# Optimization experiments

Measured on AMD Instinct MI355X. Metric: run time of the kernel, lower is better.

Reference implementation:

```python
import jax, jax.numpy as jnp
import numpy as np

RADIUS = 0.1
NSAMPLE = 32


def setup_inputs() -> dict:
    key = jax.random.key(0)
    k1, k2, k3 = jax.random.split(key, 3)
    B, N, P, C = 2, 16384, 4096, 64
    xyz = jax.random.uniform(k1, (B, N, 3), dtype=jnp.float32)
    new_xyz = jax.random.uniform(k2, (B, P, 3), dtype=jnp.float32)
    features = jax.random.normal(k3, (B, C, N), dtype=jnp.float32)
    return {"xyz": xyz, "new_xyz": new_xyz, "features": features}


def _ball_query(xyz, new_xyz, radius, nsample):
    """Return (B, npoint, nsample) int32 indices of the first `nsample` points
    (in original order) within `radius` of each query center. Slots beyond the
    number of valid neighbors are padded with the first valid index (0 if none),
    matching the standard PointNet++ CUDA ball_query semantics."""
    N = xyz.shape[1]
    # squared distances [B, P, N]
    d2 = jnp.sum((new_xyz[:, :, None, :] - xyz[:, None, :, :]) ** 2, axis=-1)
    in_ball = d2 < (radius * radius)
    # score = point index if in ball, else N (sentinel); smallest nsample scores
    # are the first nsample in-ball indices in original order.
    score = jnp.where(in_ball, jnp.arange(N, dtype=jnp.int32), jnp.int32(N))
    neg_topk, _ = jax.lax.top_k(-score, nsample)  # largest of -score == smallest score
    idx = -neg_topk  # [B, P, nsample], ascending
    first = idx[..., :1]
    idx = jnp.where(idx >= N, first, idx)  # pad invalid slots with first valid
    idx = jnp.where(idx >= N, 0, idx)      # no neighbor at all -> 0
    return idx


def _group(features, idx):
    """features (B, C, N), idx (B, P, S) -> (B, C, P, S)"""
    return jax.vmap(lambda f, i: f[:, i])(features, idx)


def reference(xyz, new_xyz, features):
    idx = _ball_query(xyz, new_xyz, RADIUS, NSAMPLE)          # (B, P, S)
    xyz_t = jnp.transpose(xyz, (0, 2, 1))                      # (B, 3, N)
    grouped_xyz = _group(xyz_t, idx)                           # (B, 3, P, S)
    grouped_xyz = grouped_xyz - jnp.transpose(new_xyz, (0, 2, 1))[..., None]
    grouped_features = _group(features, idx)                   # (B, C, P, S)
    new_features = jnp.concatenate([grouped_xyz, grouped_features], axis=1)
    return new_features
```

## Files before the change

kernel.cpp:

```cpp
#include <hip/hip_runtime.h>
#include <limits.h>

#define BB 2
#define NN 16384
#define PP 4096
#define CC 64
#define SS 32
#define R2 0.01f
#define OUTCH (3 + CC)
#define GRES 10
#define NCELL 1000

__device__ __forceinline__ int cell_of(float v) {
  int q = (int)(v * 10.0f);
  return q < 0 ? 0 : (q > GRES - 1 ? GRES - 1 : q);
}
__device__ __forceinline__ int cell_clamp_floor(float v) {
  int q = (int)floorf(v * 10.0f);
  return q < 0 ? 0 : (q > GRES - 1 ? GRES - 1 : q);
}

__global__ void zero_counters_kernel(int* hist, int* fill) {
  const int t = blockIdx.x * blockDim.x + threadIdx.x;
  if (t < BB * NCELL) { hist[t] = 0; fill[t] = 0; }
}

__global__ __launch_bounds__(256) void hist_kernel(const float* __restrict__ xyz,
                                                   int* __restrict__ hist) {
  const int i = blockIdx.x * 256 + threadIdx.x;
  const int b = i >> 14;
  const float* p = xyz + (size_t)i * 3;
  const int c = (cell_of(p[2]) * GRES + cell_of(p[1])) * GRES + cell_of(p[0]);
  atomicAdd(hist + b * NCELL + c, 1);
}

__global__ __launch_bounds__(1024) void scan_kernel(const int* __restrict__ hist,
                                                    int* __restrict__ cellStart) {
  __shared__ int sm[1024];
  const int b = blockIdx.x;
  const int t = threadIdx.x;
  const int own = (t < NCELL) ? hist[b * NCELL + t] : 0;
  sm[t] = own;
  __syncthreads();
  for (int off = 1; off < 1024; off <<= 1) {
    const int v = (t >= off) ? sm[t - off] : 0;
    __syncthreads();
    sm[t] += v;
    __syncthreads();
  }
  if (t < NCELL) cellStart[b * 1001 + t] = sm[t] - own;
  if (t == NCELL - 1) cellStart[b * 1001 + NCELL] = sm[t];
}

__global__ __launch_bounds__(256) void scatter_kernel(
    const float* __restrict__ xyz, const int* __restrict__ cellStart,
    int* __restrict__ fill, float4* __restrict__ sorted4) {
  const int i = blockIdx.x * 256 + threadIdx.x;
  const int b = i >> 14;
  const float* p = xyz + (size_t)i * 3;
  const float x = p[0], y = p[1], z = p[2];
  const int c = (cell_of(z) * GRES + cell_of(y)) * GRES + cell_of(x);
  const int r = atomicAdd(fill + b * NCELL + c, 1);
  const int pos = cellStart[b * 1001 + c] + r;
  float4 v;
  v.x = x; v.y = y; v.z = z; v.w = __int_as_float(i & (NN - 1));
  sorted4[(size_t)b * NN + pos] = v;
}

__global__ __launch_bounds__(256) void ball_query_grid(
    const float4* __restrict__ sorted4, const int* __restrict__ cellStart,
    const float* __restrict__ new_xyz, int* __restrict__ idx_out) {
#pragma clang fp contract(off)
  __shared__ unsigned bmAll[4 * 576];
  const int widx = threadIdx.x >> 6;
  const int lane = threadIdx.x & 63;
  const int wave = blockIdx.x * 4 + widx;
  const int b = wave >> 12;
  unsigned* bm = bmAll + widx * 576;

  const float cx = new_xyz[wave * 3 + 0];
  const float cy = new_xyz[wave * 3 + 1];
  const float cz = new_xyz[wave * 3 + 2];
  const float4* __restrict__ sb = sorted4 + (size_t)b * NN;
  const int* __restrict__ csb = cellStart + b * 1001;
  int* __restrict__ myout = idx_out + wave * SS;

#pragma unroll
  for (int k = 0; k < 9; ++k) bm[k * 64 + lane] = 0;

  const float mg = 0.1f + 1e-5f;
  const int lox = cell_clamp_floor(cx - mg), hix = cell_clamp_floor(cx + mg);
  const int loy = cell_clamp_floor(cy - mg), hiy = cell_clamp_floor(cy + mg);
  const int loz = cell_clamp_floor(cz - mg), hiz = cell_clamp_floor(cz + mg);
  const int nx = hix - lox + 1;

  for (int zc = loz; zc <= hiz; ++zc) {
    for (int yc = loy; yc <= hiy; ++yc) {
      const int c0 = (zc * GRES + yc) * GRES + lox;
      int s0 = __builtin_amdgcn_readfirstlane(csb[c0]);
      int e0 = __builtin_amdgcn_readfirstlane(csb[c0 + nx]);
      for (int o = s0; o < e0; o += 64) {
        const int j = o + lane;
        if (j < e0) {
          const float4 pt = sb[j];
          const float dx = cx - pt.x;
          const float dy = cy - pt.y;
          const float dz = cz - pt.z;
          const float a = dx * dx + dy * dy;
          const float d2 = a + dz * dz;
          if (d2 < R2) {
            const int orig = __float_as_int(pt.w);
            const int wi = orig >> 5;
            atomicOr(&bm[(wi >> 3) * 9 + (wi & 7)], 1u << (orig & 31));
          }
        }
      }
    }
  }
  __threadfence_block();

  unsigned w[8];
  int c = 0;
  int fi = INT_MAX;
#pragma unroll
  for (int k = 0; k < 8; ++k) {
    w[k] = bm[lane * 9 + k];
    c += (int)__popc(w[k]);
    if (fi == INT_MAX && w[k]) fi = lane * 256 + k * 32 + (int)__builtin_ctz(w[k]);
  }

  int incl = c;
#pragma unroll
  for (int d = 1; d < 64; d <<= 1) {
    const int t = __shfl_up(incl, d);
    if (lane >= d) incl += t;
  }
  const int E = incl - c;
  const int total = __shfl(incl, 63);

  const unsigned long long nb = __ballot(c > 0);
  int fc = 0;
  if (nb) fc = __shfl(fi, (int)__builtin_ctzll(nb));

  int s = E;
  if (s < SS) {
#pragma unroll
    for (int k = 0; k < 8; ++k) {
      unsigned ww = w[k];
      while (ww && s < SS) {
        const int bpos = (int)__builtin_ctz(ww);
        ww &= ww - 1;
        myout[s++] = lane * 256 + k * 32 + bpos;
      }
      if (s >= SS) break;
    }
  }
  for (int s2 = total + lane; s2 < SS; s2 += 64) myout[s2] = fc;
}

__global__ __launch_bounds__(256) void transpose_feat_kernel(
    const float* __restrict__ feat, float* __restrict__ featT) {
  __shared__ float tile[64][65];
  const int n0 = blockIdx.x * 64;
  const int b = blockIdx.y;
  const int jn = threadIdx.x & 63;
  const int g4 = threadIdx.x >> 6;

  const float* fb = feat + (size_t)b * CC * NN;
#pragma unroll
  for (int k = 0; k < 16; ++k) {
    const int c = g4 * 16 + k;
    tile[c][jn] = fb[(size_t)c * NN + n0 + jn];
  }
  __syncthreads();
  float* ft = featT + ((size_t)b * NN + n0) * CC;
#pragma unroll
  for (int k = 0; k < 16; ++k) {
    const int j = g4 * 16 + k;
    ft[(size_t)j * CC + jn] = tile[jn][j];
  }
}

#define TILE 128
__global__ __launch_bounds__(256) void group_kernel_t(
    const float* __restrict__ xyz, const float* __restrict__ new_xyz,
    const float* __restrict__ featT, const int* __restrict__ idx,
    float* __restrict__ out) {
  __shared__ float lds[TILE * 65];
  const int base = blockIdx.x * TILE;
  const int b = base >> 17;
  const int t = threadIdx.x;
  const size_t PS = (size_t)PP * SS;

  const float4* ftb = (const float4*)(featT + (size_t)b * NN * CC);
#pragma unroll
  for (int k = 0; k < 8; ++k) {
    const int u = k * 256 + t;
    const int r = u >> 4;
    const int q = u & 15;
    const int v = idx[base + r];
    const float4 val = ftb[(size_t)v * 16 + q];
    float* dst = &lds[r * 65 + q * 4];
    dst[0] = val.x; dst[1] = val.y; dst[2] = val.z; dst[3] = val.w;
  }
  __syncthreads();

  if (t < TILE) {
    const int g = base + t;
    const int v = idx[g];
    const int p = (g >> 5) & (PP - 1);
    const float* xr = xyz + ((size_t)b * NN + v) * 3;
    const float* cr = new_xyz + (size_t)(b * PP + p) * 3;
    const size_t ob = (size_t)b * OUTCH * PS + ((size_t)g & (PS - 1));
    out[ob + 0 * PS] = xr[0] - cr[0];
    out[ob + 1 * PS] = xr[1] - cr[1];
    out[ob + 2 * PS] = xr[2] - cr[2];
  }

  float* ob3 = out + (size_t)b * OUTCH * PS + 3 * PS + ((size_t)base & (PS - 1));
#pragma unroll
  for (int k = 0; k < 32; ++k) {
    const int u = k * 256 + t;
    const int c = u >> 7;
    const int r = u & 127;
    ob3[(size_t)c * PS + r] = lds[r * 65 + c];
  }
}

extern "C" void kernel_launch(void* const* d_in, const int* in_sizes, int n_in,
                              void* d_out, int out_size, void* d_ws, size_t ws_size,
                              hipStream_t stream) {
  const float* xyz = (const float*)d_in[0];
  const float* new_xyz = (const float*)d_in[1];
  const float* feat = (const float*)d_in[2];
  float* out = (float*)d_out;

  const size_t idxBytes = (size_t)BB * PP * SS * sizeof(int);
  int* idx = (int*)d_ws;
  char* ovl = (char*)d_ws + idxBytes;
  float* featT = (float*)ovl;
  float4* sorted4 = (float4*)ovl;
  int* cellStart = (int*)(ovl + (size_t)BB * NN * sizeof(float4));
  int* hist = cellStart + BB * 1001 + 2;
  int* fill = hist + BB * NCELL;

  zero_counters_kernel<<<(BB * NCELL + 255) / 256, 256, 0, stream>>>(hist, fill);
  hist_kernel<<<(BB * NN) / 256, 256, 0, stream>>>(xyz, hist);
  scan_kernel<<<BB, 1024, 0, stream>>>(hist, cellStart);
  scatter_kernel<<<(BB * NN) / 256, 256, 0, stream>>>(xyz, cellStart, fill, sorted4);
  ball_query_grid<<<(BB * PP) / 4, 256, 0, stream>>>(sorted4, cellStart, new_xyz, idx);

  transpose_feat_kernel<<<dim3(NN / 64, BB), 256, 0, stream>>>(feat, featT);
  group_kernel_t<<<(BB * PP * SS) / TILE, 256, 0, stream>>>(xyz, new_xyz, featT,
                                                            idx, out);
}
```

Before: 62.64 us.

## Fuse grid binning into one LDS kernel and flatten ball-query cell iteration

Replaces the four binning kernels (zero, histogram, scan, scatter) with a single per-batch 1024-thread kernel that builds the histogram, scan and scatter in shared memory. This removes three launches and the global atomics, at the cost of only two blocks doing the binning work. The ball query also flattens the up-to-9 cell row ranges into one linear index space via a prefix sum, so each 64-lane pass is fully used instead of each short row taking its own partially filled iteration.

```diff
diff --git a/kernel.cpp b/kernel.cpp
--- a/kernel.cpp
+++ b/kernel.cpp
@@ -20,51 +20,67 @@
   return q < 0 ? 0 : (q > GRES - 1 ? GRES - 1 : q);
 }
 
-__global__ void zero_counters_kernel(int* hist, int* fill) {
-  const int t = blockIdx.x * blockDim.x + threadIdx.x;
-  if (t < BB * NCELL) { hist[t] = 0; fill[t] = 0; }
-}
-
-__global__ __launch_bounds__(256) void hist_kernel(const float* __restrict__ xyz,
-                                                   int* __restrict__ hist) {
-  const int i = blockIdx.x * 256 + threadIdx.x;
-  const int b = i >> 14;
-  const float* p = xyz + (size_t)i * 3;
-  const int c = (cell_of(p[2]) * GRES + cell_of(p[1])) * GRES + cell_of(p[0]);
-  atomicAdd(hist + b * NCELL + c, 1);
-}
-
-__global__ __launch_bounds__(1024) void scan_kernel(const int* __restrict__ hist,
-                                                    int* __restrict__ cellStart) {
-  __shared__ int sm[1024];
+__global__ __launch_bounds__(1024) void bin_kernel(
+    const float* __restrict__ xyz, int* __restrict__ cellStartG,
+    float4* __restrict__ sorted4) {
+  __shared__ int hist[NCELL];
+  __shared__ int fill[NCELL];
+  __shared__ int cstart[NCELL];
+  __shared__ int wtot[16];
   const int b = blockIdx.x;
   const int t = threadIdx.x;
-  const int own = (t < NCELL) ? hist[b * NCELL + t] : 0;
-  sm[t] = own;
-  __syncthreads();
-  for (int off = 1; off < 1024; off <<= 1) {
-    const int v = (t >= off) ? sm[t - off] : 0;
-    __syncthreads();
-    sm[t] += v;
-    __syncthreads();
-  }
-  if (t < NCELL) cellStart[b * 1001 + t] = sm[t] - own;
-  if (t == NCELL - 1) cellStart[b * 1001 + NCELL] = sm[t];
-}
-
-__global__ __launch_bounds__(256) void scatter_kernel(
-    const float* __restrict__ xyz, const int* __restrict__ cellStart,
-    int* __restrict__ fill, float4* __restrict__ sorted4) {
-  const int i = blockIdx.x * 256 + threadIdx.x;
-  const int b = i >> 14;
-  const float* p = xyz + (size_t)i * 3;
-  const float x = p[0], y = p[1], z = p[2];
-  const int c = (cell_of(z) * GRES + cell_of(y)) * GRES + cell_of(x);
-  const int r = atomicAdd(fill + b * NCELL + c, 1);
-  const int pos = cellStart[b * 1001 + c] + r;
-  float4 v;
-  v.x = x; v.y = y; v.z = z; v.w = __int_as_float(i & (NN - 1));
-  sorted4[(size_t)b * NN + pos] = v;
+  const int lane = t & 63;
+  const int w = t >> 6;
+
+  if (t < NCELL) { hist[t] = 0; fill[t] = 0; }
+  __syncthreads();
+
+  const float* __restrict__ xb = xyz + (size_t)b * NN * 3;
+  int cells[16];
+#pragma unroll
+  for (int k = 0; k < 16; ++k) {
+    const int i = t + k * 1024;
+    const float x = xb[i * 3 + 0];
+    const float y = xb[i * 3 + 1];
+    const float z = xb[i * 3 + 2];
+    const int c = (cell_of(z) * GRES + cell_of(y)) * GRES + cell_of(x);
+    cells[k] = c;
+    atomicAdd(&hist[c], 1);
+  }
+  __syncthreads();
+
+  const int own = (t < NCELL) ? hist[t] : 0;
+  int incl = own;
+#pragma unroll
+  for (int d = 1; d < 64; d <<= 1) {
+    const int v = __shfl_up(incl, d);
+    if (lane >= d) incl += v;
+  }
+  if (lane == 63) wtot[w] = incl;
+  __syncthreads();
+  int pre = 0;
+#pragma unroll
+  for (int k = 0; k < 16; ++k) pre += (k < w) ? wtot[k] : 0;
+  const int excl = pre + incl - own;
+  if (t < NCELL) {
+    cstart[t] = excl;
+    cellStartG[b * 1001 + t] = excl;
+  }
+  if (t == 0) cellStartG[b * 1001 + NCELL] = NN;
+  __syncthreads();
+
+#pragma unroll
+  for (int k = 0; k < 16; ++k) {
+    const int i = t + k * 1024;
+    const float x = xb[i * 3 + 0];
+    const float y = xb[i * 3 + 1];
+    const float z = xb[i * 3 + 2];
+    const int c = cells[k];
+    const int r = atomicAdd(&fill[c], 1);
+    float4 v;
+    v.x = x; v.y = y; v.z = z; v.w = __int_as_float(i);
+    sorted4[(size_t)b * NN + cstart[c] + r] = v;
+  }
 }
 
 __global__ __launch_bounds__(256) void ball_query_grid(
@@ -93,50 +109,80 @@
   const int loy = cell_clamp_floor(cy - mg), hiy = cell_clamp_floor(cy + mg);
   const int loz = cell_clamp_floor(cz - mg), hiz = cell_clamp_floor(cz + mg);
   const int nx = hix - lox + 1;
-
-  for (int zc = loz; zc <= hiz; ++zc) {
-    for (int yc = loy; yc <= hiy; ++yc) {
-      const int c0 = (zc * GRES + yc) * GRES + lox;
-      int s0 = __builtin_amdgcn_readfirstlane(csb[c0]);
-      int e0 = __builtin_amdgcn_readfirstlane(csb[c0 + nx]);
-      for (int o = s0; o < e0; o += 64) {
-        const int j = o + lane;
-        if (j < e0) {
-          const float4 pt = sb[j];
-          const float dx = cx - pt.x;
-          const float dy = cy - pt.y;
-          const float dz = cz - pt.z;
-          const float a = dx * dx + dy * dy;
-          const float d2 = a + dz * dz;
-          if (d2 < R2) {
-            const int orig = __float_as_int(pt.w);
-            const int wi = orig >> 5;
-            atomicOr(&bm[(wi >> 3) * 9 + (wi & 7)], 1u << (orig & 31));
-          }
-        }
+  const int ny = hiy - loy + 1;
+  const int nz = hiz - loz + 1;
+  const int nr = nz * ny;
+
+  int s_l = 0, len_l = 0;
+  if (lane < nr) {
+    int zi, yi;
+    if (ny == 1) { zi = lane; yi = 0; }
+    else if (ny == 2) { zi = lane >> 1; yi = lane & 1; }
+    else { zi = (lane * 11) >> 5; yi = lane - zi * 3; }
+    const int c0 = ((loz + zi) * GRES + (loy + yi)) * GRES + lox;
+    s_l = csb[c0];
+    len_l = csb[c0 + nx] - s_l;
+  }
+  int incl = len_l;
+#pragma unroll
+  for (int d = 1; d <= 8; d <<= 1) {
+    const int v = __shfl_up(incl, d);
+    if (lane >= d) incl += v;
+  }
+  const int T = __shfl(incl, nr - 1);
+  const int Lx = incl - len_l;
+
+  int Lk[9], Sk[9];
+#pragma unroll
+  for (int k = 0; k < 9; ++k) {
+    Lk[k] = __shfl(Lx, k);
+    Sk[k] = __shfl(s_l, k);
+  }
+
+  for (int t0 = 0; t0 < T; t0 += 64) {
+    const int g = t0 + lane;
+    if (g < T) {
+      int L = Lk[0], S = Sk[0];
+#pragma unroll
+      for (int k = 1; k < 9; ++k) {
+        const bool cge = g >= Lk[k];
+        L = cge ? Lk[k] : L;
+        S = cge ? Sk[k] : S;
+      }
+      const float4 pt = sb[S + (g - L)];
+      const float dx = cx - pt.x;
+      const float dy = cy - pt.y;
+      const float dz = cz - pt.z;
+      const float a = dx * dx + dy * dy;
+      const float d2 = a + dz * dz;
+      if (d2 < R2) {
+        const int orig = __float_as_int(pt.w);
+        const int wi = orig >> 5;
+        atomicOr(&bm[(wi >> 3) * 9 + (wi & 7)], 1u << (orig & 31));
       }
     }
   }
   __threadfence_block();
 
-  unsigned w[8];
+  unsigned wv[8];
   int c = 0;
   int fi = INT_MAX;
 #pragma unroll
   for (int k = 0; k < 8; ++k) {
-    w[k] = bm[lane * 9 + k];
-    c += (int)__popc(w[k]);
-    if (fi == INT_MAX && w[k]) fi = lane * 256 + k * 32 + (int)__builtin_ctz(w[k]);
-  }
-
-  int incl = c;
+    wv[k] = bm[lane * 9 + k];
+    c += (int)__popc(wv[k]);
+    if (fi == INT_MAX && wv[k])
+      fi = lane * 256 + k * 32 + (int)__builtin_ctz(wv[k]);
+  }
+
+  int incl2 = c;
 #pragma unroll
   for (int d = 1; d < 64; d <<= 1) {
-    const int t = __shfl_up(incl, d);
-    if (lane >= d) incl += t;
-  }
-  const int E = incl - c;
-  const int total = __shfl(incl, 63);
+    const int t = __shfl_up(incl2, d);
+    if (lane >= d) incl2 += t;
+  }
+  const int E = incl2 - c;
+  const int total = __shfl(incl2, 63);
 
   const unsigned long long nb = __ballot(c > 0);
   int fc = 0;
@@ -146,7 +192,7 @@
   if (s < SS) {
 #pragma unroll
     for (int k = 0; k < 8; ++k) {
-      unsigned ww = w[k];
+      unsigned ww = wv[k];
       while (ww && s < SS) {
         const int bpos = (int)__builtin_ctz(ww);
         ww &= ww - 1;
@@ -241,15 +287,9 @@
   float* featT = (float*)ovl;
   float4* sorted4 = (float4*)ovl;
   int* cellStart = (int*)(ovl + (size_t)BB * NN * sizeof(float4));
-  int* hist = cellStart + BB * 1001 + 2;
-  int* fill = hist + BB * NCELL;
-
-  zero_counters_kernel<<<(BB * NCELL + 255) / 256, 256, 0, stream>>>(hist, fill);
-  hist_kernel<<<(BB * NN) / 256, 256, 0, stream>>>(xyz, hist);
-  scan_kernel<<<BB, 1024, 0, stream>>>(hist, cellStart);
-  scatter_kernel<<<(BB * NN) / 256, 256, 0, stream>>>(xyz, cellStart, fill, sorted4);
+
+  bin_kernel<<<BB, 1024, 0, stream>>>(xyz, cellStart, sorted4);
   ball_query_grid<<<(BB * PP) / 4, 256, 0, stream>>>(sorted4, cellStart, new_xyz, idx);
-
   transpose_feat_kernel<<<dim3(NN / 64, BB), 256, 0, stream>>>(feat, featT);
   group_kernel_t<<<(BB * PP * SS) / TILE, 256, 0, stream>>>(xyz, new_xyz, featT,
                                                             idx, out);
```

After: 63.29 us. Within noise of the previous version (+1.0%).
